# Performance work log

Measured on AMD Instinct MI355X. Metric: run time of the kernel, lower is better.

The kernel has to match this reference:

```python
import jax, jax.numpy as jnp
import numpy as np

B, H, S, D = 2, 16, 2048, 64


def setup_inputs() -> dict:
    key = jax.random.key(0)
    kq, kk, kv = jax.random.split(key, 3)
    q = jax.random.normal(kq, (B, H, S, D), dtype=jnp.float32)
    k = jax.random.normal(kk, (B, H, S, D), dtype=jnp.float32)
    v = jax.random.normal(kv, (B, H, S, D), dtype=jnp.float32)
    # look-ahead (causal) mask: 1 where attention is NOT allowed (future positions)
    mask = 1.0 - jnp.tril(jnp.ones((S, S), dtype=jnp.float32))
    mask = mask[None, None, :, :]  # broadcastable to (B, H, S, S)
    return {"q": q, "k": k, "v": v, "mask": mask}


def reference(q, k, v, mask):
    # scores: (B, H, Sq, Sk)
    dk = jnp.asarray(q.shape[-1], dtype=q.dtype)
    logits = jnp.einsum("bhqd,bhkd->bhqk", q, k) / jnp.sqrt(dk)
    logits = logits + mask * (-1e9)
    attn = jax.nn.softmax(logits, axis=-1)
    # dropout rate 0.0 / inference mode -> identity
    out = jnp.einsum("bhqk,bhkd->bhqd", attn, v)
    return out, attn
```

## Files before the change

### kernel.cpp

```cpp
#include <hip/hip_runtime.h>


typedef __attribute__((ext_vector_type(4))) float f32x4;
typedef __attribute__((ext_vector_type(8))) short bf16x8;

#define S_LEN 2048
#define D_DIM 64
#define LDK   72
#define SCALE 0.125f

__device__ __forceinline__ unsigned int f2bf1(float f) {
  unsigned int u = __float_as_uint(f);
  return (u + 0x7FFFu + ((u >> 16) & 1u)) >> 16;
}
__device__ __forceinline__ unsigned long long pack4bf(float a, float b, float c, float d) {
  unsigned int lo = f2bf1(a) | (f2bf1(b) << 16);
  unsigned int hi = f2bf1(c) | (f2bf1(d) << 16);
  return (unsigned long long)lo | ((unsigned long long)hi << 32);
}

__global__ __launch_bounds__(256, 2)
void attn_fused(const float* __restrict__ Qg, const float* __restrict__ Kg,
                const float* __restrict__ Vg, float* __restrict__ Og,
                float* __restrict__ Ag)
{
  __shared__ __attribute__((aligned(16))) unsigned short qs[64 * LDK];
  __shared__ __attribute__((aligned(16))) unsigned short ks[2][64 * LDK];
  __shared__ __attribute__((aligned(16))) unsigned short vs[2][64 * LDK];
  __shared__ __attribute__((aligned(16))) unsigned short ps[4 * 16 * LDK];

  const int tid  = threadIdx.x;
  const int w    = tid >> 6;
  const int l15  = tid & 15;
  const int lg   = (tid >> 4) & 3;
  const int bh   = blockIdx.x & 31;
  const int pj   = blockIdx.x >> 5;

  const float* qb = Qg + (size_t)bh * S_LEN * D_DIM;
  const float* kb = Kg + (size_t)bh * S_LEN * D_DIM;
  const float* vb = Vg + (size_t)bh * S_LEN * D_DIM;
  float* ob = Og + (size_t)bh * S_LEN * D_DIM;
  float* ab = Ag + (size_t)bh * S_LEN * S_LEN;

  unsigned short* pw = ps + w * 16 * LDK;

  for (int sel = 0; sel < 2; ++sel) {
    const int jq  = sel ? (31 - pj) : pj;
    const int q0  = jq << 6;
    const int T   = jq + 1;
    const int qr0 = q0 + w * 16 + lg * 4;

    __syncthreads();
#pragma unroll
    for (int jj = 0; jj < 4; ++jj) {
      int f = tid + jj * 256;
      int row = f >> 4, dg = f & 15;
      float4 v = *(const float4*)(qb + (q0 + row) * D_DIM + dg * 4);
      *(unsigned long long*)(qs + row * LDK + dg * 4) = pack4bf(v.x, v.y, v.z, v.w);
    }
    __syncthreads();
    const bf16x8 qf0 = *(const bf16x8*)(qs + (w * 16 + l15) * LDK + lg * 8);
    const bf16x8 qf1 = *(const bf16x8*)(qs + (w * 16 + l15) * LDK + 32 + lg * 8);

    float lsum[4] = {0.f, 0.f, 0.f, 0.f};
#pragma unroll
    for (int jj = 0; jj < 4; ++jj) {
      int f = tid + jj * 256;
      int row = f >> 4, dg = f & 15;
      float4 v = *(const float4*)(kb + row * D_DIM + dg * 4);
      *(unsigned long long*)(ks[0] + row * LDK + dg * 4) = pack4bf(v.x, v.y, v.z, v.w);
    }
    __syncthreads();
    int cur = 0;
    for (int t = 0; t < T; ++t) {
      const int kt = t << 6;
      const bool pf = (t + 1 < T);
      float4 kl[4];
      if (pf) {
#pragma unroll
        for (int jj = 0; jj < 4; ++jj) {
          int f = tid + jj * 256;
          int row = f >> 4, dg = f & 15;
          kl[jj] = *(const float4*)(kb + (kt + 64 + row) * D_DIM + dg * 4);
        }
      }
      const unsigned short* kcur = ks[cur];
#pragma unroll
      for (int kbk = 0; kbk < 4; ++kbk) {
        const bf16x8 kf0 = *(const bf16x8*)(kcur + (kbk * 16 + l15) * LDK + lg * 8);
        const bf16x8 kf1 = *(const bf16x8*)(kcur + (kbk * 16 + l15) * LDK + 32 + lg * 8);
        f32x4 s = {0.f, 0.f, 0.f, 0.f};
        s = __builtin_amdgcn_mfma_f32_16x16x32_bf16(qf0, kf0, s, 0, 0, 0);
        s = __builtin_amdgcn_mfma_f32_16x16x32_bf16(qf1, kf1, s, 0, 0, 0);
        const int kc = kt + kbk * 16 + l15;
#pragma unroll
        for (int r = 0; r < 4; ++r)
          lsum[r] += (kc <= qr0 + r) ? __expf(s[r] * SCALE) : 0.f;
      }
      if (pf) {
#pragma unroll
        for (int jj = 0; jj < 4; ++jj) {
          int f = tid + jj * 256;
          int row = f >> 4, dg = f & 15;
          *(unsigned long long*)(ks[cur ^ 1] + row * LDK + dg * 4) =
              pack4bf(kl[jj].x, kl[jj].y, kl[jj].z, kl[jj].w);
        }
      }
      __syncthreads();
      cur ^= 1;
    }
#pragma unroll
    for (int m = 1; m < 16; m <<= 1) {
#pragma unroll
      for (int r = 0; r < 4; ++r) lsum[r] += __shfl_xor(lsum[r], m, 64);
    }
    float ri[4];
#pragma unroll
    for (int r = 0; r < 4; ++r) ri[r] = 1.f / lsum[r];

    f32x4 o[4];
#pragma unroll
    for (int d = 0; d < 4; ++d) o[d] = (f32x4){0.f, 0.f, 0.f, 0.f};

#pragma unroll
    for (int jj = 0; jj < 4; ++jj) {
      int f = tid + jj * 256;
      int row = f >> 4, dg = f & 15;
      float4 v = *(const float4*)(kb + row * D_DIM + dg * 4);
      *(unsigned long long*)(ks[0] + row * LDK + dg * 4) = pack4bf(v.x, v.y, v.z, v.w);
    }
    {
      const int kb4 = tid >> 4, db4 = tid & 15;
      const float* vsrc = vb + (kb4 * 4) * D_DIM + db4 * 4;
      float4 r0 = *(const float4*)(vsrc);
      float4 r1 = *(const float4*)(vsrc + D_DIM);
      float4 r2 = *(const float4*)(vsrc + 2 * D_DIM);
      float4 r3 = *(const float4*)(vsrc + 3 * D_DIM);
      *(unsigned long long*)(vs[0] + (db4 * 4 + 0) * LDK + kb4 * 4) = pack4bf(r0.x, r1.x, r2.x, r3.x);
      *(unsigned long long*)(vs[0] + (db4 * 4 + 1) * LDK + kb4 * 4) = pack4bf(r0.y, r1.y, r2.y, r3.y);
      *(unsigned long long*)(vs[0] + (db4 * 4 + 2) * LDK + kb4 * 4) = pack4bf(r0.z, r1.z, r2.z, r3.z);
      *(unsigned long long*)(vs[0] + (db4 * 4 + 3) * LDK + kb4 * 4) = pack4bf(r0.w, r1.w, r2.w, r3.w);
    }
    __syncthreads();
    cur = 0;
    for (int t = 0; t < T; ++t) {
      const int kt = t << 6;
      const bool pf = (t + 1 < T);
      float4 kl[4], v0, v1, v2, v3;
      if (pf) {
#pragma unroll
        for (int jj = 0; jj < 4; ++jj) {
          int f = tid + jj * 256;
          int row = f >> 4, dg = f & 15;
          kl[jj] = *(const float4*)(kb + (kt + 64 + row) * D_DIM + dg * 4);
        }
        const int kb4 = tid >> 4, db4 = tid & 15;
        const float* vsrc = vb + (kt + 64 + kb4 * 4) * D_DIM + db4 * 4;
        v0 = *(const float4*)(vsrc);
        v1 = *(const float4*)(vsrc + D_DIM);
        v2 = *(const float4*)(vsrc + 2 * D_DIM);
        v3 = *(const float4*)(vsrc + 3 * D_DIM);
      }
      const unsigned short* kcur = ks[cur];
#pragma unroll
      for (int kbk = 0; kbk < 4; ++kbk) {
        const bf16x8 kf0 = *(const bf16x8*)(kcur + (kbk * 16 + l15) * LDK + lg * 8);
        const bf16x8 kf1 = *(const bf16x8*)(kcur + (kbk * 16 + l15) * LDK + 32 + lg * 8);
        f32x4 s = {0.f, 0.f, 0.f, 0.f};
        s = __builtin_amdgcn_mfma_f32_16x16x32_bf16(qf0, kf0, s, 0, 0, 0);
        s = __builtin_amdgcn_mfma_f32_16x16x32_bf16(qf1, kf1, s, 0, 0, 0);
        const int kc = kt + kbk * 16 + l15;
#pragma unroll
        for (int r = 0; r < 4; ++r) {
          float p = (kc <= qr0 + r) ? __expf(s[r] * SCALE) * ri[r] : 0.f;
          pw[(lg * 4 + r) * LDK + kbk * 16 + l15] = (unsigned short)f2bf1(p);
        }
      }
      asm volatile("s_waitcnt lgkmcnt(0)" ::: "memory");

#pragma unroll
      for (int jj = 0; jj < 4; ++jj) {
        const int row = jj * 4 + lg;
        uint2 pk2 = *(const uint2*)(pw + row * LDK + l15 * 4);
        f32x4 fv;
        fv.x = __uint_as_float((pk2.x & 0xFFFFu) << 16);
        fv.y = __uint_as_float(pk2.x & 0xFFFF0000u);
        fv.z = __uint_as_float((pk2.y & 0xFFFFu) << 16);
        fv.w = __uint_as_float(pk2.y & 0xFFFF0000u);
        __builtin_nontemporal_store(fv,
          (f32x4*)(ab + (size_t)(q0 + w * 16 + row) * S_LEN + kt + l15 * 4));
      }

      const bf16x8 pa0 = *(const bf16x8*)(pw + l15 * LDK + lg * 8);
      const bf16x8 pa1 = *(const bf16x8*)(pw + l15 * LDK + 32 + lg * 8);
      const unsigned short* vcur = vs[cur];
#pragma unroll
      for (int d = 0; d < 4; ++d) {
        const bf16x8 vf0 = *(const bf16x8*)(vcur + (d * 16 + l15) * LDK + lg * 8);
        const bf16x8 vf1 = *(const bf16x8*)(vcur + (d * 16 + l15) * LDK + 32 + lg * 8);
        o[d] = __builtin_amdgcn_mfma_f32_16x16x32_bf16(pa0, vf0, o[d], 0, 0, 0);
        o[d] = __builtin_amdgcn_mfma_f32_16x16x32_bf16(pa1, vf1, o[d], 0, 0, 0);
      }
      if (pf) {
#pragma unroll
        for (int jj = 0; jj < 4; ++jj) {
          int f = tid + jj * 256;
          int row = f >> 4, dg = f & 15;
          *(unsigned long long*)(ks[cur ^ 1] + row * LDK + dg * 4) =
              pack4bf(kl[jj].x, kl[jj].y, kl[jj].z, kl[jj].w);
        }
        const int kb4 = tid >> 4, db4 = tid & 15;
        *(unsigned long long*)(vs[cur ^ 1] + (db4 * 4 + 0) * LDK + kb4 * 4) = pack4bf(v0.x, v1.x, v2.x, v3.x);
        *(unsigned long long*)(vs[cur ^ 1] + (db4 * 4 + 1) * LDK + kb4 * 4) = pack4bf(v0.y, v1.y, v2.y, v3.y);
        *(unsigned long long*)(vs[cur ^ 1] + (db4 * 4 + 2) * LDK + kb4 * 4) = pack4bf(v0.z, v1.z, v2.z, v3.z);
        *(unsigned long long*)(vs[cur ^ 1] + (db4 * 4 + 3) * LDK + kb4 * 4) = pack4bf(v0.w, v1.w, v2.w, v3.w);
      }
      __syncthreads();
      cur ^= 1;
    }

    {
      const f32x4 z = (f32x4){0.f, 0.f, 0.f, 0.f};
#pragma unroll
      for (int jj = 0; jj < 4; ++jj) {
        const int qrow = q0 + w * 16 + jj * 4 + lg;
        float* rp = ab + (size_t)qrow * S_LEN;
        for (int c = q0 + 64 + l15 * 4; c < S_LEN; c += 64)
          __builtin_nontemporal_store(z, (f32x4*)(rp + c));
      }
    }

#pragma unroll
    for (int r = 0; r < 4; ++r) {
      float* rp = ob + (size_t)(qr0 + r) * D_DIM + l15;
      rp[0]  = o[0][r];
      rp[16] = o[1][r];
      rp[32] = o[2][r];
      rp[48] = o[3][r];
    }
  }
}

extern "C" void kernel_launch(void* const* d_in, const int* in_sizes, int n_in,
                              void* d_out, int out_size, void* d_ws, size_t ws_size,
                              hipStream_t stream) {
  (void)in_sizes; (void)n_in; (void)d_ws; (void)ws_size; (void)out_size;
  const float* q = (const float*)d_in[0];
  const float* k = (const float*)d_in[1];
  const float* v = (const float*)d_in[2];
  float* out  = (float*)d_out;
  float* attn = out + (size_t)2 * 16 * 2048 * 64;
  attn_fused<<<dim3(512), dim3(256), 0, stream>>>(q, k, v, out, attn);
}
```

Before: 144.3 us.

## Split paired query tiles into separate blocks, single-buffer K/V, raise occupancy

Each block now handles one 64-row query tile instead of a paired light/heavy pair, so the grid grows from 512 to 1024 blocks. Query tiles are assigned in a serpentine order to balance causal work. K/V shared buffers drop from double to single buffering and the P scratch reuses the Q buffer. Together these cut LDS use and let launch bounds request 3 blocks per CU. The exponent moves to exp2f with a folded log2e scale, and output stores become nontemporal. Single buffering adds extra barriers per tile and exposes load latency, which the higher occupancy is meant to hide.

```diff
diff --git a/kernel.cpp b/kernel.cpp
--- a/kernel.cpp
+++ b/kernel.cpp
@@ -7,7 +7,7 @@
 #define S_LEN 2048
 #define D_DIM 64
 #define LDK   72
-#define SCALE 0.125f
+#define SCALE2 0.18033688f
 
 __device__ __forceinline__ unsigned int f2bf1(float f) {
   unsigned int u = __float_as_uint(f);
@@ -19,22 +19,29 @@
   return (unsigned long long)lo | ((unsigned long long)hi << 32);
 }
 
-__global__ __launch_bounds__(256, 2)
+__global__ __launch_bounds__(256, 3)
 void attn_fused(const float* __restrict__ Qg, const float* __restrict__ Kg,
                 const float* __restrict__ Vg, float* __restrict__ Og,
                 float* __restrict__ Ag)
 {
   __shared__ __attribute__((aligned(16))) unsigned short qs[64 * LDK];
-  __shared__ __attribute__((aligned(16))) unsigned short ks[2][64 * LDK];
-  __shared__ __attribute__((aligned(16))) unsigned short vs[2][64 * LDK];
-  __shared__ __attribute__((aligned(16))) unsigned short ps[4 * 16 * LDK];
+  __shared__ __attribute__((aligned(16))) unsigned short ks[64 * LDK];
+  __shared__ __attribute__((aligned(16))) unsigned short vs[64 * LDK];
 
   const int tid  = threadIdx.x;
   const int w    = tid >> 6;
   const int l15  = tid & 15;
   const int lg   = (tid >> 4) & 3;
-  const int bh   = blockIdx.x & 31;
-  const int pj   = blockIdx.x >> 5;
+
+  const int b    = blockIdx.x;
+  const int bh   = b & 31;
+  const int m    = b >> 5;
+  const int s_   = m >> 3;
+  const int m0   = m & 7;
+  const int jq   = (s_ << 3) | ((s_ & 1) ? (7 - m0) : m0);
+  const int q0   = jq << 6;
+  const int T    = jq + 1;
+  const int qr0  = q0 + w * 16 + lg * 4;
 
   const float* qb = Qg + (size_t)bh * S_LEN * D_DIM;
   const float* kb = Kg + (size_t)bh * S_LEN * D_DIM;
@@ -42,202 +49,189 @@
   float* ob = Og + (size_t)bh * S_LEN * D_DIM;
   float* ab = Ag + (size_t)bh * S_LEN * S_LEN;
 
-  unsigned short* pw = ps + w * 16 * LDK;
-
-  for (int sel = 0; sel < 2; ++sel) {
-    const int jq  = sel ? (31 - pj) : pj;
-    const int q0  = jq << 6;
-    const int T   = jq + 1;
-    const int qr0 = q0 + w * 16 + lg * 4;
-
-    __syncthreads();
+#pragma unroll
+  for (int jj = 0; jj < 4; ++jj) {
+    int f = tid + jj * 256;
+    int row = f >> 4, dg = f & 15;
+    float4 v = *(const float4*)(qb + (q0 + row) * D_DIM + dg * 4);
+    *(unsigned long long*)(qs + row * LDK + dg * 4) = pack4bf(v.x, v.y, v.z, v.w);
+  }
+#pragma unroll
+  for (int jj = 0; jj < 4; ++jj) {
+    int f = tid + jj * 256;
+    int row = f >> 4, dg = f & 15;
+    float4 v = *(const float4*)(kb + row * D_DIM + dg * 4);
+    *(unsigned long long*)(ks + row * LDK + dg * 4) = pack4bf(v.x, v.y, v.z, v.w);
+  }
+  __syncthreads();
+  const bf16x8 qf0 = *(const bf16x8*)(qs + (w * 16 + l15) * LDK + lg * 8);
+  const bf16x8 qf1 = *(const bf16x8*)(qs + (w * 16 + l15) * LDK + 32 + lg * 8);
+
+  float lsum[4] = {0.f, 0.f, 0.f, 0.f};
+  for (int t = 0; t < T; ++t) {
+    const int kt = t << 6;
+    const bool pf = (t + 1 < T);
+    float4 kl[4];
+    if (pf) {
+#pragma unroll
+      for (int jj = 0; jj < 4; ++jj) {
+        int f = tid + jj * 256;
+        int row = f >> 4, dg = f & 15;
+        kl[jj] = *(const float4*)(kb + (kt + 64 + row) * D_DIM + dg * 4);
+      }
+    }
+#pragma unroll
+    for (int kbk = 0; kbk < 4; ++kbk) {
+      const bf16x8 kf0 = *(const bf16x8*)(ks + (kbk * 16 + l15) * LDK + lg * 8);
+      const bf16x8 kf1 = *(const bf16x8*)(ks + (kbk * 16 + l15) * LDK + 32 + lg * 8);
+      f32x4 s = {0.f, 0.f, 0.f, 0.f};
+      s = __builtin_amdgcn_mfma_f32_16x16x32_bf16(qf0, kf0, s, 0, 0, 0);
+      s = __builtin_amdgcn_mfma_f32_16x16x32_bf16(qf1, kf1, s, 0, 0, 0);
+      const int kc = kt + kbk * 16 + l15;
+#pragma unroll
+      for (int r = 0; r < 4; ++r)
+        lsum[r] += (kc <= qr0 + r) ? exp2f(s[r] * SCALE2) : 0.f;
+    }
+    if (pf) {
+      __syncthreads();
+#pragma unroll
+      for (int jj = 0; jj < 4; ++jj) {
+        int f = tid + jj * 256;
+        int row = f >> 4, dg = f & 15;
+        *(unsigned long long*)(ks + row * LDK + dg * 4) =
+            pack4bf(kl[jj].x, kl[jj].y, kl[jj].z, kl[jj].w);
+      }
+      __syncthreads();
+    }
+  }
+#pragma unroll
+  for (int mm = 1; mm < 16; mm <<= 1) {
+#pragma unroll
+    for (int r = 0; r < 4; ++r) lsum[r] += __shfl_xor(lsum[r], mm, 64);
+  }
+  float ri[4];
+#pragma unroll
+  for (int r = 0; r < 4; ++r) ri[r] = 1.f / lsum[r];
+
+  f32x4 o[4];
+#pragma unroll
+  for (int d = 0; d < 4; ++d) o[d] = (f32x4){0.f, 0.f, 0.f, 0.f};
+
+  unsigned short* pw = qs + w * 16 * LDK;
+
+#pragma unroll
+  for (int jj = 0; jj < 4; ++jj) {
+    int f = tid + jj * 256;
+    int row = f >> 4, dg = f & 15;
+    float4 v = *(const float4*)(kb + row * D_DIM + dg * 4);
+    *(unsigned long long*)(ks + row * LDK + dg * 4) = pack4bf(v.x, v.y, v.z, v.w);
+  }
+  {
+    const int kb4 = tid >> 4, db4 = tid & 15;
+    const float* vsrc = vb + (kb4 * 4) * D_DIM + db4 * 4;
+    float4 r0 = *(const float4*)(vsrc);
+    float4 r1 = *(const float4*)(vsrc + D_DIM);
+    float4 r2 = *(const float4*)(vsrc + 2 * D_DIM);
+    float4 r3 = *(const float4*)(vsrc + 3 * D_DIM);
+    *(unsigned long long*)(vs + (db4 * 4 + 0) * LDK + kb4 * 4) = pack4bf(r0.x, r1.x, r2.x, r3.x);
+    *(unsigned long long*)(vs + (db4 * 4 + 1) * LDK + kb4 * 4) = pack4bf(r0.y, r1.y, r2.y, r3.y);
+    *(unsigned long long*)(vs + (db4 * 4 + 2) * LDK + kb4 * 4) = pack4bf(r0.z, r1.z, r2.z, r3.z);
+    *(unsigned long long*)(vs + (db4 * 4 + 3) * LDK + kb4 * 4) = pack4bf(r0.w, r1.w, r2.w, r3.w);
+  }
+  __syncthreads();
+
+  for (int t = 0; t < T; ++t) {
+    const int kt = t << 6;
+    const bool pf = (t + 1 < T);
+    float4 kl[4], v0, v1, v2, v3;
+    if (pf) {
+#pragma unroll
+      for (int jj = 0; jj < 4; ++jj) {
+        int f = tid + jj * 256;
+        int row = f >> 4, dg = f & 15;
+        kl[jj] = *(const float4*)(kb + (kt + 64 + row) * D_DIM + dg * 4);
+      }
+      const int kb4 = tid >> 4, db4 = tid & 15;
+      const float* vsrc = vb + (kt + 64 + kb4 * 4) * D_DIM + db4 * 4;
+      v0 = *(const float4*)(vsrc);
+      v1 = *(const float4*)(vsrc + D_DIM);
+      v2 = *(const float4*)(vsrc + 2 * D_DIM);
+      v3 = *(const float4*)(vsrc + 3 * D_DIM);
+    }
+#pragma unroll
+    for (int kbk = 0; kbk < 4; ++kbk) {
+      const bf16x8 kf0 = *(const bf16x8*)(ks + (kbk * 16 + l15) * LDK + lg * 8);
+      const bf16x8 kf1 = *(const bf16x8*)(ks + (kbk * 16 + l15) * LDK + 32 + lg * 8);
+      f32x4 s = {0.f, 0.f, 0.f, 0.f};
+      s = __builtin_amdgcn_mfma_f32_16x16x32_bf16(qf0, kf0, s, 0, 0, 0);
+      s = __builtin_amdgcn_mfma_f32_16x16x32_bf16(qf1, kf1, s, 0, 0, 0);
+      const int kc = kt + kbk * 16 + l15;
+#pragma unroll
+      for (int r = 0; r < 4; ++r) {
+        float p = (kc <= qr0 + r) ? exp2f(s[r] * SCALE2) * ri[r] : 0.f;
+        pw[(lg * 4 + r) * LDK + kbk * 16 + l15] = (unsigned short)f2bf1(p);
+      }
+    }
+    asm volatile("s_waitcnt lgkmcnt(0)" ::: "memory");
+
 #pragma unroll
     for (int jj = 0; jj < 4; ++jj) {
-      int f = tid + jj * 256;
-      int row = f >> 4, dg = f & 15;
-      float4 v = *(const float4*)(qb + (q0 + row) * D_DIM + dg * 4);
-      *(unsigned long long*)(qs + row * LDK + dg * 4) = pack4bf(v.x, v.y, v.z, v.w);
-    }
-    __syncthreads();
-    const bf16x8 qf0 = *(const bf16x8*)(qs + (w * 16 + l15) * LDK + lg * 8);
-    const bf16x8 qf1 = *(const bf16x8*)(qs + (w * 16 + l15) * LDK + 32 + lg * 8);
-
-    float lsum[4] = {0.f, 0.f, 0.f, 0.f};
+      const int row = jj * 4 + lg;
+      uint2 pk2 = *(const uint2*)(pw + row * LDK + l15 * 4);
+      f32x4 fv;
+      fv.x = __uint_as_float((pk2.x & 0xFFFFu) << 16);
+      fv.y = __uint_as_float(pk2.x & 0xFFFF0000u);
+      fv.z = __uint_as_float((pk2.y & 0xFFFFu) << 16);
+      fv.w = __uint_as_float(pk2.y & 0xFFFF0000u);
+      __builtin_nontemporal_store(fv,
+        (f32x4*)(ab + (size_t)(q0 + w * 16 + row) * S_LEN + kt + l15 * 4));
+    }
+
+    const bf16x8 pa0 = *(const bf16x8*)(pw + l15 * LDK + lg * 8);
+    const bf16x8 pa1 = *(const bf16x8*)(pw + l15 * LDK + 32 + lg * 8);
+#pragma unroll
+    for (int d = 0; d < 4; ++d) {
+      const bf16x8 vf0 = *(const bf16x8*)(vs + (d * 16 + l15) * LDK + lg * 8);
+      const bf16x8 vf1 = *(const bf16x8*)(vs + (d * 16 + l15) * LDK + 32 + lg * 8);
+      o[d] = __builtin_amdgcn_mfma_f32_16x16x32_bf16(pa0, vf0, o[d], 0, 0, 0);
+      o[d] = __builtin_amdgcn_mfma_f32_16x16x32_bf16(pa1, vf1, o[d], 0, 0, 0);
+    }
+    if (pf) {
+      __syncthreads();
+#pragma unroll
+      for (int jj = 0; jj < 4; ++jj) {
+        int f = tid + jj * 256;
+        int row = f >> 4, dg = f & 15;
+        *(unsigned long long*)(ks + row * LDK + dg * 4) =
+            pack4bf(kl[jj].x, kl[jj].y, kl[jj].z, kl[jj].w);
+      }
+      const int kb4 = tid >> 4, db4 = tid & 15;
+      *(unsigned long long*)(vs + (db4 * 4 + 0) * LDK + kb4 * 4) = pack4bf(v0.x, v1.x, v2.x, v3.x);
+      *(unsigned long long*)(vs + (db4 * 4 + 1) * LDK + kb4 * 4) = pack4bf(v0.y, v1.y, v2.y, v3.y);
+      *(unsigned long long*)(vs + (db4 * 4 + 2) * LDK + kb4 * 4) = pack4bf(v0.z, v1.z, v2.z, v3.z);
+      *(unsigned long long*)(vs + (db4 * 4 + 3) * LDK + kb4 * 4) = pack4bf(v0.w, v1.w, v2.w, v3.w);
+      __syncthreads();
+    }
+  }
+
+  {
+    const f32x4 z = (f32x4){0.f, 0.f, 0.f, 0.f};
 #pragma unroll
     for (int jj = 0; jj < 4; ++jj) {
-      int f = tid + jj * 256;
-      int row = f >> 4, dg = f & 15;
-      float4 v = *(const float4*)(kb + row * D_DIM + dg * 4);
-      *(unsigned long long*)(ks[0] + row * LDK + dg * 4) = pack4bf(v.x, v.y, v.z, v.w);
-    }
-    __syncthreads();
-    int cur = 0;
-    for (int t = 0; t < T; ++t) {
-      const int kt = t << 6;
-      const bool pf = (t + 1 < T);
-      float4 kl[4];
-      if (pf) {
-#pragma unroll
-        for (int jj = 0; jj < 4; ++jj) {
-          int f = tid + jj * 256;
-          int row = f >> 4, dg = f & 15;
-          kl[jj] = *(const float4*)(kb + (kt + 64 + row) * D_DIM + dg * 4);
-        }
-      }
-      const unsigned short* kcur = ks[cur];
-#pragma unroll
-      for (int kbk = 0; kbk < 4; ++kbk) {
-        const bf16x8 kf0 = *(const bf16x8*)(kcur + (kbk * 16 + l15) * LDK + lg * 8);
-        const bf16x8 kf1 = *(const bf16x8*)(kcur + (kbk * 16 + l15) * LDK + 32 + lg * 8);
-        f32x4 s = {0.f, 0.f, 0.f, 0.f};
-        s = __builtin_amdgcn_mfma_f32_16x16x32_bf16(qf0, kf0, s, 0, 0, 0);
-        s = __builtin_amdgcn_mfma_f32_16x16x32_bf16(qf1, kf1, s, 0, 0, 0);
-        const int kc = kt + kbk * 16 + l15;
-#pragma unroll
-        for (int r = 0; r < 4; ++r)
-          lsum[r] += (kc <= qr0 + r) ? __expf(s[r] * SCALE) : 0.f;
-      }
-      if (pf) {
-#pragma unroll
-        for (int jj = 0; jj < 4; ++jj) {
-          int f = tid + jj * 256;
-          int row = f >> 4, dg = f & 15;
-          *(unsigned long long*)(ks[cur ^ 1] + row * LDK + dg * 4) =
-              pack4bf(kl[jj].x, kl[jj].y, kl[jj].z, kl[jj].w);
-        }
-      }
-      __syncthreads();
-      cur ^= 1;
-    }
-#pragma unroll
-    for (int m = 1; m < 16; m <<= 1) {
-#pragma unroll
-      for (int r = 0; r < 4; ++r) lsum[r] += __shfl_xor(lsum[r], m, 64);
-    }
-    float ri[4];
-#pragma unroll
-    for (int r = 0; r < 4; ++r) ri[r] = 1.f / lsum[r];
-
-    f32x4 o[4];
-#pragma unroll
-    for (int d = 0; d < 4; ++d) o[d] = (f32x4){0.f, 0.f, 0.f, 0.f};
-
-#pragma unroll
-    for (int jj = 0; jj < 4; ++jj) {
-      int f = tid + jj * 256;
-      int row = f >> 4, dg = f & 15;
-      float4 v = *(const float4*)(kb + row * D_DIM + dg * 4);
-      *(unsigned long long*)(ks[0] + row * LDK + dg * 4) = pack4bf(v.x, v.y, v.z, v.w);
-    }
-    {
-      const int kb4 = tid >> 4, db4 = tid & 15;
-      const float* vsrc = vb + (kb4 * 4) * D_DIM + db4 * 4;
-      float4 r0 = *(const float4*)(vsrc);
-      float4 r1 = *(const float4*)(vsrc + D_DIM);
-      float4 r2 = *(const float4*)(vsrc + 2 * D_DIM);
-      float4 r3 = *(const float4*)(vsrc + 3 * D_DIM);
-      *(unsigned long long*)(vs[0] + (db4 * 4 + 0) * LDK + kb4 * 4) = pack4bf(r0.x, r1.x, r2.x, r3.x);
-      *(unsigned long long*)(vs[0] + (db4 * 4 + 1) * LDK + kb4 * 4) = pack4bf(r0.y, r1.y, r2.y, r3.y);
-      *(unsigned long long*)(vs[0] + (db4 * 4 + 2) * LDK + kb4 * 4) = pack4bf(r0.z, r1.z, r2.z, r3.z);
-      *(unsigned long long*)(vs[0] + (db4 * 4 + 3) * LDK + kb4 * 4) = pack4bf(r0.w, r1.w, r2.w, r3.w);
-    }
-    __syncthreads();
-    cur = 0;
-    for (int t = 0; t < T; ++t) {
-      const int kt = t << 6;
-      const bool pf = (t + 1 < T);
-      float4 kl[4], v0, v1, v2, v3;
-      if (pf) {
-#pragma unroll
-        for (int jj = 0; jj < 4; ++jj) {
-          int f = tid + jj * 256;
-          int row = f >> 4, dg = f & 15;
-          kl[jj] = *(const float4*)(kb + (kt + 64 + row) * D_DIM + dg * 4);
-        }
-        const int kb4 = tid >> 4, db4 = tid & 15;
-        const float* vsrc = vb + (kt + 64 + kb4 * 4) * D_DIM + db4 * 4;
-        v0 = *(const float4*)(vsrc);
-        v1 = *(const float4*)(vsrc + D_DIM);
-        v2 = *(const float4*)(vsrc + 2 * D_DIM);
-        v3 = *(const float4*)(vsrc + 3 * D_DIM);
-      }
-      const unsigned short* kcur = ks[cur];
-#pragma unroll
-      for (int kbk = 0; kbk < 4; ++kbk) {
-        const bf16x8 kf0 = *(const bf16x8*)(kcur + (kbk * 16 + l15) * LDK + lg * 8);
-        const bf16x8 kf1 = *(const bf16x8*)(kcur + (kbk * 16 + l15) * LDK + 32 + lg * 8);
-        f32x4 s = {0.f, 0.f, 0.f, 0.f};
-        s = __builtin_amdgcn_mfma_f32_16x16x32_bf16(qf0, kf0, s, 0, 0, 0);
-        s = __builtin_amdgcn_mfma_f32_16x16x32_bf16(qf1, kf1, s, 0, 0, 0);
-        const int kc = kt + kbk * 16 + l15;
-#pragma unroll
-        for (int r = 0; r < 4; ++r) {
-          float p = (kc <= qr0 + r) ? __expf(s[r] * SCALE) * ri[r] : 0.f;
-          pw[(lg * 4 + r) * LDK + kbk * 16 + l15] = (unsigned short)f2bf1(p);
-        }
-      }
-      asm volatile("s_waitcnt lgkmcnt(0)" ::: "memory");
-
-#pragma unroll
-      for (int jj = 0; jj < 4; ++jj) {
-        const int row = jj * 4 + lg;
-        uint2 pk2 = *(const uint2*)(pw + row * LDK + l15 * 4);
-        f32x4 fv;
-        fv.x = __uint_as_float((pk2.x & 0xFFFFu) << 16);
-        fv.y = __uint_as_float(pk2.x & 0xFFFF0000u);
-        fv.z = __uint_as_float((pk2.y & 0xFFFFu) << 16);
-        fv.w = __uint_as_float(pk2.y & 0xFFFF0000u);
-        __builtin_nontemporal_store(fv,
-          (f32x4*)(ab + (size_t)(q0 + w * 16 + row) * S_LEN + kt + l15 * 4));
-      }
-
-      const bf16x8 pa0 = *(const bf16x8*)(pw + l15 * LDK + lg * 8);
-      const bf16x8 pa1 = *(const bf16x8*)(pw + l15 * LDK + 32 + lg * 8);
-      const unsigned short* vcur = vs[cur];
-#pragma unroll
-      for (int d = 0; d < 4; ++d) {
-        const bf16x8 vf0 = *(const bf16x8*)(vcur + (d * 16 + l15) * LDK + lg * 8);
-        const bf16x8 vf1 = *(const bf16x8*)(vcur + (d * 16 + l15) * LDK + 32 + lg * 8);
-        o[d] = __builtin_amdgcn_mfma_f32_16x16x32_bf16(pa0, vf0, o[d], 0, 0, 0);
-        o[d] = __builtin_amdgcn_mfma_f32_16x16x32_bf16(pa1, vf1, o[d], 0, 0, 0);
-      }
-      if (pf) {
-#pragma unroll
-        for (int jj = 0; jj < 4; ++jj) {
-          int f = tid + jj * 256;
-          int row = f >> 4, dg = f & 15;
-          *(unsigned long long*)(ks[cur ^ 1] + row * LDK + dg * 4) =
-              pack4bf(kl[jj].x, kl[jj].y, kl[jj].z, kl[jj].w);
-        }
-        const int kb4 = tid >> 4, db4 = tid & 15;
-        *(unsigned long long*)(vs[cur ^ 1] + (db4 * 4 + 0) * LDK + kb4 * 4) = pack4bf(v0.x, v1.x, v2.x, v3.x);
-        *(unsigned long long*)(vs[cur ^ 1] + (db4 * 4 + 1) * LDK + kb4 * 4) = pack4bf(v0.y, v1.y, v2.y, v3.y);
-        *(unsigned long long*)(vs[cur ^ 1] + (db4 * 4 + 2) * LDK + kb4 * 4) = pack4bf(v0.z, v1.z, v2.z, v3.z);
-        *(unsigned long long*)(vs[cur ^ 1] + (db4 * 4 + 3) * LDK + kb4 * 4) = pack4bf(v0.w, v1.w, v2.w, v3.w);
-      }
-      __syncthreads();
-      cur ^= 1;
-    }
-
-    {
-      const f32x4 z = (f32x4){0.f, 0.f, 0.f, 0.f};
-#pragma unroll
-      for (int jj = 0; jj < 4; ++jj) {
-        const int qrow = q0 + w * 16 + jj * 4 + lg;
-        float* rp = ab + (size_t)qrow * S_LEN;
-        for (int c = q0 + 64 + l15 * 4; c < S_LEN; c += 64)
-          __builtin_nontemporal_store(z, (f32x4*)(rp + c));
-      }
-    }
-
-#pragma unroll
-    for (int r = 0; r < 4; ++r) {
-      float* rp = ob + (size_t)(qr0 + r) * D_DIM + l15;
-      rp[0]  = o[0][r];
-      rp[16] = o[1][r];
-      rp[32] = o[2][r];
-      rp[48] = o[3][r];
-    }
+      const int qrow = q0 + w * 16 + jj * 4 + lg;
+      float* rp = ab + (size_t)qrow * S_LEN;
+      for (int c = q0 + 64 + l15 * 4; c < S_LEN; c += 64)
+        __builtin_nontemporal_store(z, (f32x4*)(rp + c));
+    }
+  }
+
+#pragma unroll
+  for (int r = 0; r < 4; ++r) {
+    float* rp = ob + (size_t)(qr0 + r) * D_DIM + l15;
+    __builtin_nontemporal_store(o[0][r], rp);
+    __builtin_nontemporal_store(o[1][r], rp + 16);
+    __builtin_nontemporal_store(o[2][r], rp + 32);
+    __builtin_nontemporal_store(o[3][r], rp + 48);
   }
 }
 
@@ -250,5 +244,5 @@
   const float* v = (const float*)d_in[2];
   float* out  = (float*)d_out;
   float* attn = out + (size_t)2 * 16 * 2048 * 64;
-  attn_fused<<<dim3(512), dim3(256), 0, stream>>>(q, k, v, out, attn);
-}
+  attn_fused<<<dim3(1024), dim3(256), 0, stream>>>(q, k, v, out, attn);
+}
```

Result: slower. 153.1 us (+6.1%).

## Interleave zero-fill of masked attention tiles into pass one and specialize masked tiles

Applied to the files above, without the earlier changes.

The zero-fill of the upper-triangular attention region moves from a separate tail loop into the first (row-sum) pass, one 64-column tile per iteration, so those stores overlap with compute. The causal mask comparison now runs only on the diagonal tile in both passes. __expf with a 0.125 scale becomes exp2f with a log2e-folded scale. Output stores become nontemporal. An extra barrier is added before the K/V reload, and the first loop may run more iterations than needed for compute, which adds branch overhead.

```diff
diff --git a/kernel.cpp b/kernel.cpp
--- a/kernel.cpp
+++ b/kernel.cpp
@@ -7,7 +7,7 @@
 #define S_LEN 2048
 #define D_DIM 64
 #define LDK   72
-#define SCALE 0.125f
+#define SCALE2 0.18033688f
 
 __device__ __forceinline__ unsigned int f2bf1(float f) {
   unsigned int u = __float_as_uint(f);
@@ -48,6 +48,7 @@
     const int jq  = sel ? (31 - pj) : pj;
     const int q0  = jq << 6;
     const int T   = jq + 1;
+    const int NF  = 31 - jq;
     const int qr0 = q0 + w * 16 + lg * 4;
 
     __syncthreads();
@@ -72,42 +73,61 @@
     }
     __syncthreads();
     int cur = 0;
-    for (int t = 0; t < T; ++t) {
-      const int kt = t << 6;
-      const bool pf = (t + 1 < T);
+
+#define P1_KBK(MASKED)                                                          \
+    _Pragma("unroll")                                                           \
+    for (int kbk = 0; kbk < 4; ++kbk) {                                         \
+      const bf16x8 kf0 = *(const bf16x8*)(kcur + (kbk * 16 + l15) * LDK + lg * 8);      \
+      const bf16x8 kf1 = *(const bf16x8*)(kcur + (kbk * 16 + l15) * LDK + 32 + lg * 8); \
+      f32x4 s = {0.f, 0.f, 0.f, 0.f};                                           \
+      s = __builtin_amdgcn_mfma_f32_16x16x32_bf16(qf0, kf0, s, 0, 0, 0);        \
+      s = __builtin_amdgcn_mfma_f32_16x16x32_bf16(qf1, kf1, s, 0, 0, 0);        \
+      const int kc = kt + kbk * 16 + l15;                                       \
+      _Pragma("unroll")                                                         \
+      for (int r = 0; r < 4; ++r) {                                             \
+        float e = exp2f(s[r] * SCALE2);                                         \
+        if (MASKED) lsum[r] += (kc <= qr0 + r) ? e : 0.f;                       \
+        else        lsum[r] += e;                                               \
+      }                                                                         \
+    }
+
+    for (int t = 0; t < 32; ++t) {
+      if (t >= T && t >= NF) break;
+      const bool cmp = (t < T);
+      const bool pf  = (t + 1 < T);
       float4 kl[4];
       if (pf) {
 #pragma unroll
         for (int jj = 0; jj < 4; ++jj) {
           int f = tid + jj * 256;
           int row = f >> 4, dg = f & 15;
-          kl[jj] = *(const float4*)(kb + (kt + 64 + row) * D_DIM + dg * 4);
-        }
-      }
-      const unsigned short* kcur = ks[cur];
-#pragma unroll
-      for (int kbk = 0; kbk < 4; ++kbk) {
-        const bf16x8 kf0 = *(const bf16x8*)(kcur + (kbk * 16 + l15) * LDK + lg * 8);
-        const bf16x8 kf1 = *(const bf16x8*)(kcur + (kbk * 16 + l15) * LDK + 32 + lg * 8);
-        f32x4 s = {0.f, 0.f, 0.f, 0.f};
-        s = __builtin_amdgcn_mfma_f32_16x16x32_bf16(qf0, kf0, s, 0, 0, 0);
-        s = __builtin_amdgcn_mfma_f32_16x16x32_bf16(qf1, kf1, s, 0, 0, 0);
-        const int kc = kt + kbk * 16 + l15;
-#pragma unroll
-        for (int r = 0; r < 4; ++r)
-          lsum[r] += (kc <= qr0 + r) ? __expf(s[r] * SCALE) : 0.f;
-      }
-      if (pf) {
-#pragma unroll
-        for (int jj = 0; jj < 4; ++jj) {
-          int f = tid + jj * 256;
-          int row = f >> 4, dg = f & 15;
-          *(unsigned long long*)(ks[cur ^ 1] + row * LDK + dg * 4) =
-              pack4bf(kl[jj].x, kl[jj].y, kl[jj].z, kl[jj].w);
-        }
-      }
-      __syncthreads();
-      cur ^= 1;
+          kl[jj] = *(const float4*)(kb + (((t + 1) << 6) + row) * D_DIM + dg * 4);
+        }
+      }
+      if (t < NF) {
+        const f32x4 z = (f32x4){0.f, 0.f, 0.f, 0.f};
+        const int cf = S_LEN - ((t + 1) << 6) + (tid & 15) * 4;
+        float* rp0 = ab + (size_t)(q0 + (tid >> 4)) * S_LEN + cf;
+#pragma unroll
+        for (int i = 0; i < 4; ++i)
+          __builtin_nontemporal_store(z, (f32x4*)(rp0 + (size_t)(16 * i) * S_LEN));
+      }
+      if (cmp) {
+        const int kt = t << 6;
+        const unsigned short* kcur = ks[cur];
+        if (t == T - 1) { P1_KBK(1) } else { P1_KBK(0) }
+        if (pf) {
+#pragma unroll
+          for (int jj = 0; jj < 4; ++jj) {
+            int f = tid + jj * 256;
+            int row = f >> 4, dg = f & 15;
+            *(unsigned long long*)(ks[cur ^ 1] + row * LDK + dg * 4) =
+                pack4bf(kl[jj].x, kl[jj].y, kl[jj].z, kl[jj].w);
+          }
+        }
+        __syncthreads();
+        cur ^= 1;
+      }
     }
 #pragma unroll
     for (int m = 1; m < 16; m <<= 1) {
@@ -122,6 +142,7 @@
 #pragma unroll
     for (int d = 0; d < 4; ++d) o[d] = (f32x4){0.f, 0.f, 0.f, 0.f};
 
+    __syncthreads();
 #pragma unroll
     for (int jj = 0; jj < 4; ++jj) {
       int f = tid + jj * 256;
@@ -142,6 +163,24 @@
       *(unsigned long long*)(vs[0] + (db4 * 4 + 3) * LDK + kb4 * 4) = pack4bf(r0.w, r1.w, r2.w, r3.w);
     }
     __syncthreads();
+
+#define P2_KBK(MASKED)                                                          \
+    _Pragma("unroll")                                                           \
+    for (int kbk = 0; kbk < 4; ++kbk) {                                         \
+      const bf16x8 kf0 = *(const bf16x8*)(kcur + (kbk * 16 + l15) * LDK + lg * 8);      \
+      const bf16x8 kf1 = *(const bf16x8*)(kcur + (kbk * 16 + l15) * LDK + 32 + lg * 8); \
+      f32x4 s = {0.f, 0.f, 0.f, 0.f};                                           \
+      s = __builtin_amdgcn_mfma_f32_16x16x32_bf16(qf0, kf0, s, 0, 0, 0);        \
+      s = __builtin_amdgcn_mfma_f32_16x16x32_bf16(qf1, kf1, s, 0, 0, 0);        \
+      const int kc = kt + kbk * 16 + l15;                                       \
+      _Pragma("unroll")                                                         \
+      for (int r = 0; r < 4; ++r) {                                             \
+        float p = exp2f(s[r] * SCALE2) * ri[r];                                 \
+        if (MASKED) p = (kc <= qr0 + r) ? p : 0.f;                              \
+        pw[(lg * 4 + r) * LDK + kbk * 16 + l15] = (unsigned short)f2bf1(p);     \
+      }                                                                         \
+    }
+
     cur = 0;
     for (int t = 0; t < T; ++t) {
       const int kt = t << 6;
@@ -162,20 +201,7 @@
         v3 = *(const float4*)(vsrc + 3 * D_DIM);
       }
       const unsigned short* kcur = ks[cur];
-#pragma unroll
-      for (int kbk = 0; kbk < 4; ++kbk) {
-        const bf16x8 kf0 = *(const bf16x8*)(kcur + (kbk * 16 + l15) * LDK + lg * 8);
-        const bf16x8 kf1 = *(const bf16x8*)(kcur + (kbk * 16 + l15) * LDK + 32 + lg * 8);
-        f32x4 s = {0.f, 0.f, 0.f, 0.f};
-        s = __builtin_amdgcn_mfma_f32_16x16x32_bf16(qf0, kf0, s, 0, 0, 0);
-        s = __builtin_amdgcn_mfma_f32_16x16x32_bf16(qf1, kf1, s, 0, 0, 0);
-        const int kc = kt + kbk * 16 + l15;
-#pragma unroll
-        for (int r = 0; r < 4; ++r) {
-          float p = (kc <= qr0 + r) ? __expf(s[r] * SCALE) * ri[r] : 0.f;
-          pw[(lg * 4 + r) * LDK + kbk * 16 + l15] = (unsigned short)f2bf1(p);
-        }
-      }
+      if (t == T - 1) { P2_KBK(1) } else { P2_KBK(0) }
       asm volatile("s_waitcnt lgkmcnt(0)" ::: "memory");
 
 #pragma unroll
@@ -219,24 +245,13 @@
       cur ^= 1;
     }
 
-    {
-      const f32x4 z = (f32x4){0.f, 0.f, 0.f, 0.f};
-#pragma unroll
-      for (int jj = 0; jj < 4; ++jj) {
-        const int qrow = q0 + w * 16 + jj * 4 + lg;
-        float* rp = ab + (size_t)qrow * S_LEN;
-        for (int c = q0 + 64 + l15 * 4; c < S_LEN; c += 64)
-          __builtin_nontemporal_store(z, (f32x4*)(rp + c));
-      }
-    }
-
 #pragma unroll
     for (int r = 0; r < 4; ++r) {
       float* rp = ob + (size_t)(qr0 + r) * D_DIM + l15;
-      rp[0]  = o[0][r];
-      rp[16] = o[1][r];
-      rp[32] = o[2][r];
-      rp[48] = o[3][r];
+      __builtin_nontemporal_store(o[0][r], rp);
+      __builtin_nontemporal_store(o[1][r], rp + 16);
+      __builtin_nontemporal_store(o[2][r], rp + 32);
+      __builtin_nontemporal_store(o[3][r], rp + 48);
     }
   }
 }
```

Result: slower. 161.9 us (+12.2%).

## Transpose score MFMA to write attn directly, reuse Q smem, exp2 and unmasked fast path

Applied to the files above, without the earlier changes.

Swaps the MFMA operand order so each lane holds four consecutive key columns of one query row. Attention probabilities can then be stored straight to global as f32x4 without the LDS round-trip and bf16 truncation, and P is packed to LDS once for the PV MFMA. The P buffer now aliases the Q staging buffer, which removes a shared array and one barrier. Masking is applied only on the diagonal tile, exp uses exp2f with a prescaled log2e constant, and the row-sum reduction shrinks to two shuffles. Output stores become nontemporal.

```diff
diff --git a/kernel.cpp b/kernel.cpp
--- a/kernel.cpp
+++ b/kernel.cpp
@@ -7,7 +7,7 @@
 #define S_LEN 2048
 #define D_DIM 64
 #define LDK   72
-#define SCALE 0.125f
+#define SCALE2 0.18033688f
 
 __device__ __forceinline__ unsigned int f2bf1(float f) {
   unsigned int u = __float_as_uint(f);
@@ -27,7 +27,6 @@
   __shared__ __attribute__((aligned(16))) unsigned short qs[64 * LDK];
   __shared__ __attribute__((aligned(16))) unsigned short ks[2][64 * LDK];
   __shared__ __attribute__((aligned(16))) unsigned short vs[2][64 * LDK];
-  __shared__ __attribute__((aligned(16))) unsigned short ps[4 * 16 * LDK];
 
   const int tid  = threadIdx.x;
   const int w    = tid >> 6;
@@ -42,13 +41,14 @@
   float* ob = Og + (size_t)bh * S_LEN * D_DIM;
   float* ab = Ag + (size_t)bh * S_LEN * S_LEN;
 
-  unsigned short* pw = ps + w * 16 * LDK;
+  unsigned short* pw = qs + w * 16 * LDK;
 
   for (int sel = 0; sel < 2; ++sel) {
-    const int jq  = sel ? (31 - pj) : pj;
-    const int q0  = jq << 6;
-    const int T   = jq + 1;
-    const int qr0 = q0 + w * 16 + lg * 4;
+    const int jq   = sel ? (31 - pj) : pj;
+    const int q0   = jq << 6;
+    const int T    = jq + 1;
+    const int qrow = q0 + w * 16 + l15;
+    const int qr0  = q0 + w * 16 + lg * 4;
 
     __syncthreads();
 #pragma unroll
@@ -58,11 +58,6 @@
       float4 v = *(const float4*)(qb + (q0 + row) * D_DIM + dg * 4);
       *(unsigned long long*)(qs + row * LDK + dg * 4) = pack4bf(v.x, v.y, v.z, v.w);
     }
-    __syncthreads();
-    const bf16x8 qf0 = *(const bf16x8*)(qs + (w * 16 + l15) * LDK + lg * 8);
-    const bf16x8 qf1 = *(const bf16x8*)(qs + (w * 16 + l15) * LDK + 32 + lg * 8);
-
-    float lsum[4] = {0.f, 0.f, 0.f, 0.f};
 #pragma unroll
     for (int jj = 0; jj < 4; ++jj) {
       int f = tid + jj * 256;
@@ -71,7 +66,28 @@
       *(unsigned long long*)(ks[0] + row * LDK + dg * 4) = pack4bf(v.x, v.y, v.z, v.w);
     }
     __syncthreads();
+    const bf16x8 qf0 = *(const bf16x8*)(qs + (w * 16 + l15) * LDK + lg * 8);
+    const bf16x8 qf1 = *(const bf16x8*)(qs + (w * 16 + l15) * LDK + 32 + lg * 8);
+
+    float lsum = 0.f;
     int cur = 0;
+
+#define P1_KBK(MASKED)                                                                  \
+    _Pragma("unroll")                                                                   \
+    for (int kbk = 0; kbk < 4; ++kbk) {                                                 \
+      const bf16x8 kf0 = *(const bf16x8*)(kcur + (kbk * 16 + l15) * LDK + lg * 8);      \
+      const bf16x8 kf1 = *(const bf16x8*)(kcur + (kbk * 16 + l15) * LDK + 32 + lg * 8); \
+      f32x4 s = {0.f, 0.f, 0.f, 0.f};                                                   \
+      s = __builtin_amdgcn_mfma_f32_16x16x32_bf16(kf0, qf0, s, 0, 0, 0);                \
+      s = __builtin_amdgcn_mfma_f32_16x16x32_bf16(kf1, qf1, s, 0, 0, 0);                \
+      _Pragma("unroll")                                                                 \
+      for (int r = 0; r < 4; ++r) {                                                     \
+        float e = exp2f(s[r] * SCALE2);                                                 \
+        if (MASKED) lsum += (kt + kbk * 16 + lg * 4 + r <= qrow) ? e : 0.f;             \
+        else        lsum += e;                                                          \
+      }                                                                                 \
+    }
+
     for (int t = 0; t < T; ++t) {
       const int kt = t << 6;
       const bool pf = (t + 1 < T);
@@ -85,18 +101,7 @@
         }
       }
       const unsigned short* kcur = ks[cur];
-#pragma unroll
-      for (int kbk = 0; kbk < 4; ++kbk) {
-        const bf16x8 kf0 = *(const bf16x8*)(kcur + (kbk * 16 + l15) * LDK + lg * 8);
-        const bf16x8 kf1 = *(const bf16x8*)(kcur + (kbk * 16 + l15) * LDK + 32 + lg * 8);
-        f32x4 s = {0.f, 0.f, 0.f, 0.f};
-        s = __builtin_amdgcn_mfma_f32_16x16x32_bf16(qf0, kf0, s, 0, 0, 0);
-        s = __builtin_amdgcn_mfma_f32_16x16x32_bf16(qf1, kf1, s, 0, 0, 0);
-        const int kc = kt + kbk * 16 + l15;
-#pragma unroll
-        for (int r = 0; r < 4; ++r)
-          lsum[r] += (kc <= qr0 + r) ? __expf(s[r] * SCALE) : 0.f;
-      }
+      if (t == T - 1) { P1_KBK(1) } else { P1_KBK(0) }
       if (pf) {
 #pragma unroll
         for (int jj = 0; jj < 4; ++jj) {
@@ -109,14 +114,9 @@
       __syncthreads();
       cur ^= 1;
     }
-#pragma unroll
-    for (int m = 1; m < 16; m <<= 1) {
-#pragma unroll
-      for (int r = 0; r < 4; ++r) lsum[r] += __shfl_xor(lsum[r], m, 64);
-    }
-    float ri[4];
-#pragma unroll
-    for (int r = 0; r < 4; ++r) ri[r] = 1.f / lsum[r];
+    lsum += __shfl_xor(lsum, 16, 64);
+    lsum += __shfl_xor(lsum, 32, 64);
+    const float ri = 1.f / lsum;
 
     f32x4 o[4];
 #pragma unroll
@@ -142,6 +142,28 @@
       *(unsigned long long*)(vs[0] + (db4 * 4 + 3) * LDK + kb4 * 4) = pack4bf(r0.w, r1.w, r2.w, r3.w);
     }
     __syncthreads();
+
+#define P2_KBK(MASKED)                                                                  \
+    _Pragma("unroll")                                                                   \
+    for (int kbk = 0; kbk < 4; ++kbk) {                                                 \
+      const bf16x8 kf0 = *(const bf16x8*)(kcur + (kbk * 16 + l15) * LDK + lg * 8);      \
+      const bf16x8 kf1 = *(const bf16x8*)(kcur + (kbk * 16 + l15) * LDK + 32 + lg * 8); \
+      f32x4 s = {0.f, 0.f, 0.f, 0.f};                                                   \
+      s = __builtin_amdgcn_mfma_f32_16x16x32_bf16(kf0, qf0, s, 0, 0, 0);                \
+      s = __builtin_amdgcn_mfma_f32_16x16x32_bf16(kf1, qf1, s, 0, 0, 0);                \
+      f32x4 pv;                                                                         \
+      _Pragma("unroll")                                                                 \
+      for (int r = 0; r < 4; ++r) {                                                     \
+        float p = exp2f(s[r] * SCALE2) * ri;                                            \
+        if (MASKED) p = (kt + kbk * 16 + lg * 4 + r <= qrow) ? p : 0.f;                 \
+        pv[r] = p;                                                                      \
+      }                                                                                 \
+      __builtin_nontemporal_store(pv,                                                   \
+        (f32x4*)(ab + (size_t)qrow * S_LEN + kt + kbk * 16 + lg * 4));                  \
+      *(unsigned long long*)(pw + l15 * LDK + kbk * 16 + lg * 4) =                      \
+          pack4bf(pv[0], pv[1], pv[2], pv[3]);                                          \
+    }
+
     cur = 0;
     for (int t = 0; t < T; ++t) {
       const int kt = t << 6;
@@ -162,34 +184,8 @@
         v3 = *(const float4*)(vsrc + 3 * D_DIM);
       }
       const unsigned short* kcur = ks[cur];
-#pragma unroll
-      for (int kbk = 0; kbk < 4; ++kbk) {
-        const bf16x8 kf0 = *(const bf16x8*)(kcur + (kbk * 16 + l15) * LDK + lg * 8);
-        const bf16x8 kf1 = *(const bf16x8*)(kcur + (kbk * 16 + l15) * LDK + 32 + lg * 8);
-        f32x4 s = {0.f, 0.f, 0.f, 0.f};
-        s = __builtin_amdgcn_mfma_f32_16x16x32_bf16(qf0, kf0, s, 0, 0, 0);
-        s = __builtin_amdgcn_mfma_f32_16x16x32_bf16(qf1, kf1, s, 0, 0, 0);
-        const int kc = kt + kbk * 16 + l15;
-#pragma unroll
-        for (int r = 0; r < 4; ++r) {
-          float p = (kc <= qr0 + r) ? __expf(s[r] * SCALE) * ri[r] : 0.f;
-          pw[(lg * 4 + r) * LDK + kbk * 16 + l15] = (unsigned short)f2bf1(p);
-        }
-      }
+      if (t == T - 1) { P2_KBK(1) } else { P2_KBK(0) }
       asm volatile("s_waitcnt lgkmcnt(0)" ::: "memory");
-
-#pragma unroll
-      for (int jj = 0; jj < 4; ++jj) {
-        const int row = jj * 4 + lg;
-        uint2 pk2 = *(const uint2*)(pw + row * LDK + l15 * 4);
-        f32x4 fv;
-        fv.x = __uint_as_float((pk2.x & 0xFFFFu) << 16);
-        fv.y = __uint_as_float(pk2.x & 0xFFFF0000u);
-        fv.z = __uint_as_float((pk2.y & 0xFFFFu) << 16);
-        fv.w = __uint_as_float(pk2.y & 0xFFFF0000u);
-        __builtin_nontemporal_store(fv,
-          (f32x4*)(ab + (size_t)(q0 + w * 16 + row) * S_LEN + kt + l15 * 4));
-      }
 
       const bf16x8 pa0 = *(const bf16x8*)(pw + l15 * LDK + lg * 8);
       const bf16x8 pa1 = *(const bf16x8*)(pw + l15 * LDK + 32 + lg * 8);
@@ -223,8 +219,8 @@
       const f32x4 z = (f32x4){0.f, 0.f, 0.f, 0.f};
 #pragma unroll
       for (int jj = 0; jj < 4; ++jj) {
-        const int qrow = q0 + w * 16 + jj * 4 + lg;
-        float* rp = ab + (size_t)qrow * S_LEN;
+        const int zrow = q0 + w * 16 + jj * 4 + lg;
+        float* rp = ab + (size_t)zrow * S_LEN;
         for (int c = q0 + 64 + l15 * 4; c < S_LEN; c += 64)
           __builtin_nontemporal_store(z, (f32x4*)(rp + c));
       }
@@ -233,10 +229,10 @@
 #pragma unroll
     for (int r = 0; r < 4; ++r) {
       float* rp = ob + (size_t)(qr0 + r) * D_DIM + l15;
-      rp[0]  = o[0][r];
-      rp[16] = o[1][r];
-      rp[32] = o[2][r];
-      rp[48] = o[3][r];
+      __builtin_nontemporal_store(o[0][r], rp);
+      __builtin_nontemporal_store(o[1][r], rp + 16);
+      __builtin_nontemporal_store(o[2][r], rp + 32);
+      __builtin_nontemporal_store(o[3][r], rp + 48);
     }
   }
 }
```

New measurement: 170.3 us. 1.18x slower.
